# Kernel tuning notes

Measured on AMD Instinct MI355X. Metric: run time of the kernel, lower is better.

## Reference

```python
import jax, jax.numpy as jnp
import numpy as np

B, GNN_DIM, TR_DIM, F = 16384, 512, 768, 1024


def setup_inputs() -> dict:
    key = jax.random.key(0)
    ks = jax.random.split(key, 16)
    s = 0.02
    return {
        "gnn_features": jax.random.normal(ks[0], (B, GNN_DIM), jnp.float32),
        "transformer_features": jax.random.normal(ks[1], (B, TR_DIM), jnp.float32),
        # gnn_projector / transformer_projector (torch Linear: y = x @ W.T + b)
        "Wg": jax.random.normal(ks[2], (F, GNN_DIM), jnp.float32) * s,
        "bg": jnp.zeros((F,), jnp.float32),
        "Wt": jax.random.normal(ks[3], (F, TR_DIM), jnp.float32) * s,
        "bt": jnp.zeros((F,), jnp.float32),
        # MultiheadAttention value-projection slice of in_proj_weight and out_proj.
        # With seq_len==1 the softmax over a single key is identically 1, so the
        # attention output is exactly out_proj(v_proj(key)); Q/K projections do
        # not affect the output (their gradients are exactly zero).
        "Wv": jax.random.normal(ks[4], (F, F), jnp.float32) * s,
        "bv": jnp.zeros((F,), jnp.float32),
        "Wo": jax.random.normal(ks[5], (F, F), jnp.float32) * s,
        "bo": jnp.zeros((F,), jnp.float32),
        # fusion_layers: Linear(2F -> F), GELU, Dropout(eval: identity), Linear(F -> F)
        "W1": jax.random.normal(ks[6], (F, 2 * F), jnp.float32) * s,
        "b1": jnp.zeros((F,), jnp.float32),
        "W2": jax.random.normal(ks[7], (F, F), jnp.float32) * s,
        "b2": jnp.zeros((F,), jnp.float32),
    }


def reference(gnn_features, transformer_features, Wg, bg, Wt, bt, Wv, bv, Wo, bo, W1, b1, W2, b2):
    # projections to fusion space  [B, F]
    gnn_proj = gnn_features @ Wg.T + bg
    tr_proj = transformer_features @ Wt.T + bt
    # degenerate single-token cross-attention: softmax over 1 key == 1, so
    # attn(q, k, v=k) = out_proj(v_proj(k)) regardless of the query.
    gnn_attended = (tr_proj @ Wv.T + bv) @ Wo.T + bo   # attention(gnn_seq, tr_seq, tr_seq)
    tr_attended = (gnn_proj @ Wv.T + bv) @ Wo.T + bo   # attention(tr_seq, gnn_seq, gnn_seq)
    combined = jnp.concatenate([gnn_attended, tr_attended], axis=-1)  # [B, 2F]
    h = jax.nn.gelu(combined @ W1.T + b1, approximate=False)          # exact GELU (torch default)
    fused = h @ W2.T + b2
    return fused + gnn_proj + tr_proj
```

## Files before the change

### kernel.cpp

```cpp
#include <hip/hip_runtime.h>
#include <cmath>

#define GAS __attribute__((address_space(1)))
#define LAS __attribute__((address_space(3)))

typedef __bf16 bf16x8 __attribute__((ext_vector_type(8)));
typedef float f32x4 __attribute__((ext_vector_type(4)));

__device__ __forceinline__ void gload16(const void* g, void* l) {
    __builtin_amdgcn_global_load_lds((const GAS void*)g, (LAS void*)l, 16, 0, 0);
}

__global__ void k_prep_convert(const float* __restrict__ gnn, const float* __restrict__ tr,
                               const float* __restrict__ Wo, const float* __restrict__ W1,
                               const float* __restrict__ W2, const float* __restrict__ Wg,
                               const float* __restrict__ Wt,
                               __bf16* __restrict__ X, __bf16* __restrict__ Wo_b,
                               __bf16* __restrict__ W1ab, __bf16* __restrict__ Wp) {
    int b = blockIdx.x;
    const float* src; __bf16* dst; int sld, dld, base, c8;
    if (b < 4096)       { src = gnn;       sld = 512;  dst = X + 1024;        dld = 2304; base = 0;     c8 = 64; }
    else if (b < 10240) { src = tr;        sld = 768;  dst = X + 1536;        dld = 2304; base = 4096;  c8 = 96; }
    else if (b < 10752) { src = Wo;        sld = 1024; dst = Wo_b;            dld = 1024; base = 10240; c8 = 128; }
    else if (b < 11264) { src = W1;        sld = 2048; dst = W1ab;            dld = 1024; base = 10752; c8 = 128; }
    else if (b < 11776) { src = W1 + 1024; sld = 2048; dst = W1ab + 1024*1024; dld = 1024; base = 11264; c8 = 128; }
    else if (b < 12288) { src = W2;        sld = 1024; dst = Wp;              dld = 2304; base = 11776; c8 = 128; }
    else if (b < 12544) { src = Wg;        sld = 512;  dst = Wp + 1024;       dld = 2304; base = 12288; c8 = 64; }
    else                { src = Wt;        sld = 768;  dst = Wp + 1536;       dld = 2304; base = 12544; c8 = 96; }
    int idx = (b - base) * 256 + threadIdx.x;
    int r = idx / c8;
    int c = (idx - r * c8) << 3;
    const float4* s = reinterpret_cast<const float4*>(src + (long)r * sld + c);
    float4 x0 = s[0], x1 = s[1];
    bf16x8 v;
    v[0] = (__bf16)x0.x; v[1] = (__bf16)x0.y; v[2] = (__bf16)x0.z; v[3] = (__bf16)x0.w;
    v[4] = (__bf16)x1.x; v[5] = (__bf16)x1.y; v[6] = (__bf16)x1.z; v[7] = (__bf16)x1.w;
    *reinterpret_cast<bf16x8*>(dst + (long)r * dld + c) = v;
}

__global__ void k_prep_transpose(const float* __restrict__ Wv, const float* __restrict__ Wg,
                                 const float* __restrict__ Wt,
                                 __bf16* __restrict__ WvT, __bf16* __restrict__ WgT,
                                 __bf16* __restrict__ WtT) {
    __shared__ float t[32][33];
    int b = blockIdx.x;
    const float* src; __bf16* dst; int R, C, tile;
    if (b < 1024)      { src = Wv; dst = WvT; R = 1024; C = 1024; tile = b; }
    else if (b < 1536) { src = Wg; dst = WgT; R = 1024; C = 512;  tile = b - 1024; }
    else               { src = Wt; dst = WtT; R = 1024; C = 768;  tile = b - 1536; }
    int tx_n = C >> 5;
    int c0 = (tile % tx_n) << 5, r0 = (tile / tx_n) << 5;
    int tx = threadIdx.x, ty = threadIdx.y;
    #pragma unroll
    for (int i = 0; i < 32; i += 8)
        t[ty + i][tx] = src[(long)(r0 + ty + i) * C + c0 + tx];
    __syncthreads();
    #pragma unroll
    for (int i = 0; i < 32; i += 8)
        dst[(long)(c0 + ty + i) * R + r0 + tx] = (__bf16)t[tx][ty + i];
}

__global__ void k_bias_att(const float* __restrict__ Wo, const float* __restrict__ bv,
                           const float* __restrict__ bo, float* __restrict__ b_att) {
    int i = blockIdx.x;
    float s = 0.f;
    for (int k = threadIdx.x; k < 1024; k += 256) s += Wo[i * 1024 + k] * bv[k];
    __shared__ float red[256];
    red[threadIdx.x] = s;
    __syncthreads();
    for (int off = 128; off > 0; off >>= 1) {
        if (threadIdx.x < off) red[threadIdx.x] += red[threadIdx.x + off];
        __syncthreads();
    }
    if (threadIdx.x == 0) b_att[i] = red[0] + bo[i];
}

__global__ void k_bias_z2(const float* __restrict__ W1, const float* __restrict__ b_att,
                          const float* __restrict__ b1,
                          const __bf16* __restrict__ P, const __bf16* __restrict__ Q,
                          const float* __restrict__ bt, const float* __restrict__ bg,
                          const float* __restrict__ b2,
                          float* __restrict__ bz2, float* __restrict__ b_out) {
    int i = blockIdx.x;
    float s = 0.f;
    for (int k = threadIdx.x; k < 1024; k += 256) {
        s += (W1[(long)i * 2048 + k] + W1[(long)i * 2048 + 1024 + k]) * b_att[k];
        s += (float)P[i * 1024 + k] * bt[k];
        s += (float)Q[i * 1024 + k] * bg[k];
    }
    __shared__ float red[256];
    red[threadIdx.x] = s;
    __syncthreads();
    for (int off = 128; off > 0; off >>= 1) {
        if (threadIdx.x < off) red[threadIdx.x] += red[threadIdx.x + off];
        __syncthreads();
    }
    if (threadIdx.x == 0) {
        bz2[i] = red[0] + b1[i];
        b_out[i] = b2[i] + bg[i] + bt[i];
    }
}

template <int BM, int BN>
__global__ __launch_bounds__(256, 2) void k_gemm_nt(
    const __bf16* __restrict__ A, int lda,
    const __bf16* __restrict__ B, int ldb,
    __bf16* __restrict__ C, int ldc,
    int K, int n_tiles) {
    constexpr int BK = 32;
    constexpr int MR = BM / 32, NR = BN / 32;
    __shared__ alignas(16) __bf16 As[2][BM][BK];
    __shared__ alignas(16) __bf16 Bs[2][BN][BK];

    const int tid = threadIdx.x;
    const int lane = tid & 63;
    const int wave = tid >> 6;
    int bid = blockIdx.x;
    const int nwg = gridDim.x;
    if ((nwg & 7) == 0) bid = (bid & 7) * (nwg >> 3) + (bid >> 3);
    const int bn = bid % n_tiles;
    const int bm = bid / n_tiles;
    const int m0 = bm * BM, n0 = bn * BN;

    const int rp_l = tid >> 2;
    const int sp = tid & 3;

    const int wr = (wave >> 1) * (BM / 2);
    const int wc = (wave & 1) * (BN / 2);
    const int fr = lane & 15;
    const int fb = (lane >> 4) << 4;

    f32x4 acc[MR][NR] = {};
    const int nk = K / BK;

    auto stage = [&](int buf, int kt) {
        char* abase = (char*)&As[buf][0][0];
        char* bbase = (char*)&Bs[buf][0][0];
        #pragma unroll
        for (int it = 0; it < BM / 64; ++it) {
            int rp = it * 64 + rp_l;
            int rl = (rp & ~1) | ((rp ^ (rp >> 2)) & 1);
            int sl = sp ^ (rl & 3);
            gload16(A + (long)(m0 + rl) * lda + kt * BK + sl * 8,
                    abase + it * 4096 + tid * 16);
        }
        #pragma unroll
        for (int it = 0; it < BN / 64; ++it) {
            int rp = it * 64 + rp_l;
            int rl = (rp & ~1) | ((rp ^ (rp >> 2)) & 1);
            int sl = sp ^ (rl & 3);
            gload16(B + (long)(n0 + rl) * ldb + kt * BK + sl * 8,
                    bbase + it * 4096 + tid * 16);
        }
    };

    stage(0, 0);
    for (int kt = 0; kt < nk; ++kt) {
        const int buf = kt & 1;
        __syncthreads();
        if (kt + 1 < nk) stage(buf ^ 1, kt + 1);
        const char* abase = (const char*)&As[buf][0][0];
        const char* bbase = (const char*)&Bs[buf][0][0];
        bf16x8 af[MR], bfr[NR];
        #pragma unroll
        for (int m = 0; m < MR; ++m) {
            int r = wr + m * 16 + fr;
            af[m] = *(const bf16x8*)(abase + (((r << 6) + fb) ^ ((r & 7) << 4)));
        }
        #pragma unroll
        for (int n = 0; n < NR; ++n) {
            int r = wc + n * 16 + fr;
            bfr[n] = *(const bf16x8*)(bbase + (((r << 6) + fb) ^ ((r & 7) << 4)));
        }
        #pragma unroll
        for (int m = 0; m < MR; ++m)
            #pragma unroll
            for (int n = 0; n < NR; ++n)
                acc[m][n] = __builtin_amdgcn_mfma_f32_16x16x32_bf16(af[m], bfr[n], acc[m][n], 0, 0, 0);
    }

    const int r0 = (lane >> 4) << 2;
    #pragma unroll
    for (int n = 0; n < NR; ++n) {
        const int gc = n0 + wc + n * 16 + fr;
        #pragma unroll
        for (int m = 0; m < MR; ++m) {
            const long rbase = (long)(m0 + wr + m * 16 + r0);
            #pragma unroll
            for (int r = 0; r < 4; ++r)
                C[(rbase + r) * ldc + gc] = (__bf16)acc[m][n][r];
        }
    }
}

template <int MODE>
__device__ __forceinline__ void gemm8_body(
    const __bf16* __restrict__ A, int lda,
    const __bf16* __restrict__ B, int ldb,
    void* __restrict__ Cv, int ldc,
    const float* __restrict__ bias,
    int K, int n_tiles) {
    __shared__ __bf16 As[2][2][256][32];
    __shared__ __bf16 Bs[2][2][256][32];

    const int tid = threadIdx.x;
    const int lane = tid & 63;
    const int wave = tid >> 6;
    const int wm = wave >> 2;
    const int wn = wave & 3;

    int bid = blockIdx.x;
    const int nwg = gridDim.x;
    if ((nwg & 7) == 0) bid = (bid & 7) * (nwg >> 3) + (bid >> 3);
    const int bn = bid % n_tiles;
    const int bm = bid / n_tiles;
    const int m0 = bm * 256, n0 = bn * 256;

    const int rp0 = tid >> 2;
    const int rl0 = (rp0 & ~1) | ((rp0 ^ (rp0 >> 2)) & 1);
    const int slo = (tid & 3) ^ (rl0 & 3);
    const __bf16* Ag = A + (long)(m0 + rl0) * lda + slo * 8;
    const __bf16* Bg = B + (long)(n0 + rl0) * ldb + slo * 8;
    const long lda128 = (long)128 * lda;
    const long ldb128 = (long)128 * ldb;
    const int tid16 = tid * 16;

    const int fr = lane & 15;
    const int gb = (lane >> 4) << 4;

    f32x4 acc[8][4] = {};
    bf16x8 af[2][4];
    bf16x8 bfr[2][4];

    const int nk = K >> 6;
    const int NI = nk >> 1;

#define STAGE_A(PAR, KT, KH) { \
        char* l_ = (char*)&As[PAR][KH][0][0] + tid16; \
        const __bf16* g_ = Ag + (long)(KT) * 64 + (KH) * 32; \
        gload16(g_, l_); \
        gload16(g_ + lda128, l_ + 8192); }
#define STAGE_B(PAR, KT, KH) { \
        char* l_ = (char*)&Bs[PAR][KH][0][0] + tid16; \
        const __bf16* g_ = Bg + (long)(KT) * 64 + (KH) * 32; \
        gload16(g_, l_); \
        gload16(g_ + ldb128, l_ + 8192); }
#define VMC6 asm volatile("s_waitcnt vmcnt(6)" ::: "memory")
#define VMC4 asm volatile("s_waitcnt vmcnt(4)" ::: "memory")
#define VMC0 asm volatile("s_waitcnt vmcnt(0)" ::: "memory")
#define BAR  __builtin_amdgcn_s_barrier()
#define PIN  __builtin_amdgcn_sched_barrier(0)
#define RD_A(IDX, PAR, KS, MH) { \
        const char* a_ = (const char*)&As[PAR][KS][0][0]; \
        _Pragma("unroll") \
        for (int m_ = 0; m_ < 4; ++m_) { \
            int r_ = wm * 128 + (MH) * 64 + m_ * 16 + fr; \
            af[IDX][m_] = *(const bf16x8*)(a_ + (((r_ << 6) + gb) ^ ((r_ & 7) << 4))); } }
#define RD_B(IDX, PAR, KS) { \
        const char* b_ = (const char*)&Bs[PAR][KS][0][0]; \
        _Pragma("unroll") \
        for (int n_ = 0; n_ < 4; ++n_) { \
            int r_ = wn * 64 + n_ * 16 + fr; \
            bfr[IDX][n_] = *(const bf16x8*)(b_ + (((r_ << 6) + gb) ^ ((r_ & 7) << 4))); } }
#define MFMA16(AC, BC, MH) { \
        __builtin_amdgcn_s_setprio(1); \
        _Pragma("unroll") \
        for (int m_ = 0; m_ < 4; ++m_) { \
            _Pragma("unroll") \
            for (int n_ = 0; n_ < 4; ++n_) \
                acc[(MH) * 4 + m_][n_] = __builtin_amdgcn_mfma_f32_16x16x32_bf16( \
                    af[AC][m_], bfr[BC][n_], acc[(MH) * 4 + m_][n_], 0, 0, 0); } \
        __builtin_amdgcn_s_setprio(0); }

    STAGE_B(0, 0, 0); STAGE_A(0, 0, 0); STAGE_B(0, 0, 1); STAGE_A(0, 0, 1);
    STAGE_B(1, 1, 0); STAGE_A(1, 1, 0); STAGE_B(1, 1, 1);
    VMC4;
    BAR;
    RD_B(0, 0, 0); RD_A(0, 0, 0, 0);

    for (int I = 0; I < NI; ++I) {
        const int t = 2 * I;
        const bool nl = (I < NI - 1);
        STAGE_A(1, t + 1, 1);
        BAR; PIN; RD_A(1, 0, 0, 1); PIN;            MFMA16(0, 0, 0); BAR;
        if (nl) STAGE_B(0, t + 2, 0);
        BAR; PIN; RD_B(1, 0, 1); RD_A(0, 0, 1, 0); PIN; MFMA16(1, 0, 1); BAR;
        if (nl) STAGE_A(0, t + 2, 0);
        BAR; PIN; RD_A(1, 0, 1, 1); PIN;            MFMA16(0, 1, 0); BAR;
        if (nl) { STAGE_B(0, t + 2, 1); VMC6; } else { VMC0; }
        BAR; PIN; RD_B(0, 1, 0); RD_A(0, 1, 0, 0); PIN; MFMA16(1, 1, 1); BAR;
        if (nl) STAGE_A(0, t + 2, 1);
        BAR; PIN; RD_A(1, 1, 0, 1); PIN;            MFMA16(0, 0, 0); BAR;
        if (nl) STAGE_B(1, t + 3, 0);
        BAR; PIN; RD_B(1, 1, 1); RD_A(0, 1, 1, 0); PIN; MFMA16(1, 0, 1); BAR;
        if (nl) STAGE_A(1, t + 3, 0);
        BAR; PIN; RD_A(1, 1, 1, 1); PIN;            MFMA16(0, 1, 0); BAR;
        if (nl) { STAGE_B(1, t + 3, 1); VMC6; }
        BAR; PIN; RD_B(0, 0, 0); RD_A(0, 0, 0, 0); PIN; MFMA16(1, 1, 1); BAR;
    }
#undef MFMA16
#undef RD_B
#undef RD_A
#undef PIN
#undef BAR
#undef VMC0
#undef VMC4
#undef VMC6
#undef STAGE_B
#undef STAGE_A

    const int r0q = (lane >> 4) << 2;
    #pragma unroll
    for (int n = 0; n < 4; ++n) {
        const int gc = n0 + wn * 64 + n * 16 + fr;
        const float bval = bias ? bias[gc] : 0.0f;
        #pragma unroll
        for (int mq = 0; mq < 8; ++mq) {
            const long rbase = (long)(m0 + wm * 128 + mq * 16 + r0q);
            #pragma unroll
            for (int r = 0; r < 4; ++r) {
                float v = acc[mq][n][r] + bval;
                const long row = rbase + r;
                if (MODE == 1) {
                    float u = v * (0.7978845608f + 0.0356774081f * v * v);
                    float e = __expf(-2.0f * fabsf(u));
                    float th = (1.0f - e) / (1.0f + e);
                    th = copysignf(th, u);
                    v = 0.5f * v * (1.0f + th);
                    ((__bf16*)Cv)[row * ldc + gc] = (__bf16)v;
                } else {
                    ((float*)Cv)[row * ldc + gc] = v;
                }
            }
        }
    }
}

__global__ __launch_bounds__(512, 2) void k_gemm8_gelu(
    const __bf16* __restrict__ A, int lda, const __bf16* __restrict__ B, int ldb,
    void* __restrict__ Cv, int ldc, const float* __restrict__ bias, int K, int n_tiles) {
    gemm8_body<1>(A, lda, B, ldb, Cv, ldc, bias, K, n_tiles);
}
__global__ __launch_bounds__(512, 2) void k_gemm8_out(
    const __bf16* __restrict__ A, int lda, const __bf16* __restrict__ B, int ldb,
    void* __restrict__ Cv, int ldc, const float* __restrict__ bias, int K, int n_tiles) {
    gemm8_body<2>(A, lda, B, ldb, Cv, ldc, bias, K, n_tiles);
}

extern "C" void kernel_launch(void* const* d_in, const int* in_sizes, int n_in,
                              void* d_out, int out_size, void* d_ws, size_t ws_size,
                              hipStream_t stream) {
    constexpr int Bsz = 16384, F = 1024, GD = 512, TD = 768;
    constexpr int XLD = F + GD + TD;

    const float* gnn = (const float*)d_in[0];
    const float* tr  = (const float*)d_in[1];
    const float* Wg  = (const float*)d_in[2];
    const float* bg  = (const float*)d_in[3];
    const float* Wt  = (const float*)d_in[4];
    const float* bt  = (const float*)d_in[5];
    const float* Wv  = (const float*)d_in[6];
    const float* bv  = (const float*)d_in[7];
    const float* Wo  = (const float*)d_in[8];
    const float* bo  = (const float*)d_in[9];
    const float* W1  = (const float*)d_in[10];
    const float* b1  = (const float*)d_in[11];
    const float* W2  = (const float*)d_in[12];
    const float* b2  = (const float*)d_in[13];
    float* out = (float*)d_out;

    char* w = (char*)d_ws;
    auto alloc = [&](size_t bytes) {
        char* p = w;
        w += (bytes + 255) & ~(size_t)255;
        return p;
    };
    __bf16* X    = (__bf16*)alloc((size_t)Bsz * XLD * 2);
    __bf16* M1   = (__bf16*)alloc((size_t)F * (GD + TD) * 2);
    __bf16* Wp   = (__bf16*)alloc((size_t)F * XLD * 2);
    __bf16* WvT  = (__bf16*)alloc((size_t)F * F * 2);
    __bf16* WgT  = (__bf16*)alloc((size_t)GD * F * 2);
    __bf16* WtT  = (__bf16*)alloc((size_t)TD * F * 2);
    __bf16* Wo_b = (__bf16*)alloc((size_t)F * F * 2);
    __bf16* W1ab = (__bf16*)alloc((size_t)2 * F * F * 2);
    __bf16* AT   = (__bf16*)alloc((size_t)F * F * 2);
    __bf16* PQ   = (__bf16*)alloc((size_t)2 * F * F * 2);
    float* b_att = (float*)alloc(F * 4);
    float* bz2   = (float*)alloc(F * 4);
    float* b_out = (float*)alloc(F * 4);
    if ((size_t)(w - (char*)d_ws) > ws_size) return;

    dim3 b256(256);
    __bf16* P = PQ;
    __bf16* Q = PQ + (size_t)F * F;

    k_prep_convert<<<dim3(12928), b256, 0, stream>>>(gnn, tr, Wo, W1, W2, Wg, Wt,
                                                     X, Wo_b, W1ab, Wp);
    k_prep_transpose<<<dim3(2304), dim3(32, 8), 0, stream>>>(Wv, Wg, Wt, WvT, WgT, WtT);
    k_bias_att<<<dim3(F), b256, 0, stream>>>(Wo, bv, bo, b_att);

    k_gemm_nt<64, 64><<<dim3((F / 64) * (F / 64)), b256, 0, stream>>>(
        WvT, F, Wo_b, F, AT, F, F, F / 64);
    k_gemm_nt<64, 64><<<dim3((2 * F / 64) * (F / 64)), b256, 0, stream>>>(
        W1ab, F, AT, F, PQ, F, F, F / 64);
    k_gemm_nt<64, 64><<<dim3((F / 64) * (GD / 64)), b256, 0, stream>>>(
        Q, F, WgT, F, M1, GD + TD, F, GD / 64);
    k_gemm_nt<64, 64><<<dim3((F / 64) * (TD / 64)), b256, 0, stream>>>(
        P, F, WtT, F, M1 + GD, GD + TD, F, TD / 64);

    k_bias_z2<<<dim3(F), b256, 0, stream>>>(W1, b_att, b1, P, Q, bt, bg, b2, bz2, b_out);

    k_gemm8_gelu<<<dim3((Bsz / 256) * (F / 256)), dim3(512), 0, stream>>>(
        X + F, XLD, M1, GD + TD, X, XLD, bz2, GD + TD, F / 256);

    k_gemm8_out<<<dim3((Bsz / 256) * (F / 256)), dim3(512), 0, stream>>>(
        X, XLD, Wp, XLD, out, F, b_out, XLD, F / 256);
}
```

Measured before the change: 233.0 us.

## Restructure gemm8 LDS layout, staging schedule, and vectorize epilogue through LDS

```diff
diff --git a/kernel.cpp b/kernel.cpp
--- a/kernel.cpp
+++ b/kernel.cpp
@@ -200,8 +200,7 @@
     void* __restrict__ Cv, int ldc,
     const float* __restrict__ bias,
     int K, int n_tiles) {
-    __shared__ __bf16 As[2][2][256][32];
-    __shared__ __bf16 Bs[2][2][256][32];
+    __shared__ char lds[131072];
 
     const int tid = threadIdx.x;
     const int lane = tid & 63;
@@ -216,123 +215,144 @@
     const int bm = bid / n_tiles;
     const int m0 = bm * 256, n0 = bn * 256;
 
-    const int rp0 = tid >> 2;
-    const int rl0 = (rp0 & ~1) | ((rp0 ^ (rp0 >> 2)) & 1);
-    const int slo = (tid & 3) ^ (rl0 & 3);
-    const __bf16* Ag = A + (long)(m0 + rl0) * lda + slo * 8;
-    const __bf16* Bg = B + (long)(n0 + rl0) * ldb + slo * 8;
-    const long lda128 = (long)128 * lda;
-    const long ldb128 = (long)128 * ldb;
+    const int rowA = ((tid >> 7) << 4) + (tid & 15);
+    const int colA = (((tid >> 6) & 1) << 5) + (((tid >> 4) & 3) << 3);
+    const int rowB = ((tid >> 6) << 4) + (tid & 15);
+    const int colB = (((tid >> 4) & 3) << 3);
+    const __bf16* Ag = A + (long)(m0 + rowA) * lda + colA;
+    const __bf16* Bg = B + (long)(n0 + rowB) * ldb + colB;
     const int tid16 = tid * 16;
-
+    const int l16 = lane * 16;
     const int fr = lane & 15;
-    const int gb = (lane >> 4) << 4;
+
+    const int bnh = wn >> 1;
+    const int bno = (wn & 1) * 4096;
 
     f32x4 acc[8][4] = {};
-    bf16x8 af[2][4];
+    bf16x8 af[4];
     bf16x8 bfr[2][4];
 
     const int nk = K >> 6;
     const int NI = nk >> 1;
 
-#define STAGE_A(PAR, KT, KH) { \
-        char* l_ = (char*)&As[PAR][KH][0][0] + tid16; \
-        const __bf16* g_ = Ag + (long)(KT) * 64 + (KH) * 32; \
-        gload16(g_, l_); \
-        gload16(g_ + lda128, l_ + 8192); }
-#define STAGE_B(PAR, KT, KH) { \
-        char* l_ = (char*)&Bs[PAR][KH][0][0] + tid16; \
-        const __bf16* g_ = Bg + (long)(KT) * 64 + (KH) * 32; \
-        gload16(g_, l_); \
-        gload16(g_ + ldb128, l_ + 8192); }
+#define STAGE_A(PAR, KT, MH, QH) \
+    gload16(Ag + (long)(KT) * 64 + (long)((MH) * 128 + (QH) * 64) * lda, \
+            lds + (PAR) * 32768 + (MH) * 16384 + (QH) * 8192 + tid16)
+#define STAGE_B(PAR, KT, NH, KK) \
+    gload16(Bg + (long)(KT) * 64 + (KK) * 32 + (long)((NH) * 128) * ldb, \
+            lds + 65536 + (PAR) * 32768 + (NH) * 16384 + (KK) * 8192 + tid16)
+#define VMC8 asm volatile("s_waitcnt vmcnt(8)" ::: "memory")
 #define VMC6 asm volatile("s_waitcnt vmcnt(6)" ::: "memory")
-#define VMC4 asm volatile("s_waitcnt vmcnt(4)" ::: "memory")
 #define VMC0 asm volatile("s_waitcnt vmcnt(0)" ::: "memory")
 #define BAR  __builtin_amdgcn_s_barrier()
-#define PIN  __builtin_amdgcn_sched_barrier(0)
-#define RD_A(IDX, PAR, KS, MH) { \
-        const char* a_ = (const char*)&As[PAR][KS][0][0]; \
+#define RD_A4(PAR, QH, KK) { \
+        const char* a_ = lds + (PAR) * 32768 + wm * 16384 + (QH) * 8192 + (KK) * 1024; \
         _Pragma("unroll") \
-        for (int m_ = 0; m_ < 4; ++m_) { \
-            int r_ = wm * 128 + (MH) * 64 + m_ * 16 + fr; \
-            af[IDX][m_] = *(const bf16x8*)(a_ + (((r_ << 6) + gb) ^ ((r_ & 7) << 4))); } }
-#define RD_B(IDX, PAR, KS) { \
-        const char* b_ = (const char*)&Bs[PAR][KS][0][0]; \
+        for (int m_ = 0; m_ < 4; ++m_) \
+            af[m_] = *(const bf16x8*)(a_ + m_ * 2048 + l16); }
+#define RD_B4(KK, PAR) { \
+        const char* b_ = lds + 65536 + (PAR) * 32768 + bnh * 16384 + (KK) * 8192 + bno; \
         _Pragma("unroll") \
-        for (int n_ = 0; n_ < 4; ++n_) { \
-            int r_ = wn * 64 + n_ * 16 + fr; \
-            bfr[IDX][n_] = *(const bf16x8*)(b_ + (((r_ << 6) + gb) ^ ((r_ & 7) << 4))); } }
-#define MFMA16(AC, BC, MH) { \
+        for (int n_ = 0; n_ < 4; ++n_) \
+            bfr[KK][n_] = *(const bf16x8*)(b_ + n_ * 1024 + l16); }
+#define MFMA16(QH, KK) { \
         __builtin_amdgcn_s_setprio(1); \
         _Pragma("unroll") \
         for (int m_ = 0; m_ < 4; ++m_) { \
             _Pragma("unroll") \
             for (int n_ = 0; n_ < 4; ++n_) \
-                acc[(MH) * 4 + m_][n_] = __builtin_amdgcn_mfma_f32_16x16x32_bf16( \
-                    af[AC][m_], bfr[BC][n_], acc[(MH) * 4 + m_][n_], 0, 0, 0); } \
+                acc[(QH) * 4 + m_][n_] = __builtin_amdgcn_mfma_f32_16x16x32_bf16( \
+                    af[m_], bfr[KK][n_], acc[(QH) * 4 + m_][n_], 0, 0, 0); } \
         __builtin_amdgcn_s_setprio(0); }
 
-    STAGE_B(0, 0, 0); STAGE_A(0, 0, 0); STAGE_B(0, 0, 1); STAGE_A(0, 0, 1);
-    STAGE_B(1, 1, 0); STAGE_A(1, 1, 0); STAGE_B(1, 1, 1);
-    VMC4;
-    BAR;
-    RD_B(0, 0, 0); RD_A(0, 0, 0, 0);
+    STAGE_A(0, 0, 0, 0); STAGE_A(0, 0, 1, 0);
+    STAGE_B(0, 0, 0, 0); STAGE_B(0, 0, 1, 0);
+    STAGE_A(0, 0, 0, 1); STAGE_A(0, 0, 1, 1);
+    STAGE_B(0, 0, 0, 1); STAGE_B(0, 0, 1, 1);
+    STAGE_A(1, 1, 0, 0); STAGE_A(1, 1, 1, 0);
+    STAGE_B(1, 1, 0, 0); STAGE_B(1, 1, 1, 0);
 
     for (int I = 0; I < NI; ++I) {
         const int t = 2 * I;
-        const bool nl = (I < NI - 1);
-        STAGE_A(1, t + 1, 1);
-        BAR; PIN; RD_A(1, 0, 0, 1); PIN;            MFMA16(0, 0, 0); BAR;
-        if (nl) STAGE_B(0, t + 2, 0);
-        BAR; PIN; RD_B(1, 0, 1); RD_A(0, 0, 1, 0); PIN; MFMA16(1, 0, 1); BAR;
-        if (nl) STAGE_A(0, t + 2, 0);
-        BAR; PIN; RD_A(1, 0, 1, 1); PIN;            MFMA16(0, 1, 0); BAR;
-        if (nl) { STAGE_B(0, t + 2, 1); VMC6; } else { VMC0; }
-        BAR; PIN; RD_B(0, 1, 0); RD_A(0, 1, 0, 0); PIN; MFMA16(1, 1, 1); BAR;
-        if (nl) STAGE_A(0, t + 2, 1);
-        BAR; PIN; RD_A(1, 1, 0, 1); PIN;            MFMA16(0, 0, 0); BAR;
-        if (nl) STAGE_B(1, t + 3, 0);
-        BAR; PIN; RD_B(1, 1, 1); RD_A(0, 1, 1, 0); PIN; MFMA16(1, 0, 1); BAR;
-        if (nl) STAGE_A(1, t + 3, 0);
-        BAR; PIN; RD_A(1, 1, 1, 1); PIN;            MFMA16(0, 1, 0); BAR;
-        if (nl) { STAGE_B(1, t + 3, 1); VMC6; }
-        BAR; PIN; RD_B(0, 0, 0); RD_A(0, 0, 0, 0); PIN; MFMA16(1, 1, 1); BAR;
+        const bool nl = (I + 1 < NI);
+        VMC8;
+        STAGE_A(1, t + 1, 0, 1); STAGE_A(1, t + 1, 1, 1);
+        BAR; RD_B4(0, 0); RD_A4(0, 0, 0); MFMA16(0, 0); BAR;
+        VMC6;
+        STAGE_B(1, t + 1, 0, 1); STAGE_B(1, t + 1, 1, 1);
+        BAR; RD_B4(1, 0); RD_A4(0, 0, 1); MFMA16(0, 1); BAR;
+        if (nl) { STAGE_A(0, t + 2, 0, 0); STAGE_A(0, t + 2, 1, 0); } else { VMC0; }
+        BAR; RD_A4(0, 1, 0); MFMA16(1, 0); BAR;
+        if (nl) { STAGE_B(0, t + 2, 0, 0); STAGE_B(0, t + 2, 1, 0); }
+        BAR; RD_A4(0, 1, 1); MFMA16(1, 1); BAR;
+        VMC8;
+        if (nl) { STAGE_A(0, t + 2, 0, 1); STAGE_A(0, t + 2, 1, 1); }
+        BAR; RD_B4(0, 1); RD_A4(1, 0, 0); MFMA16(0, 0); BAR;
+        VMC6;
+        if (nl) { STAGE_B(0, t + 2, 0, 1); STAGE_B(0, t + 2, 1, 1); }
+        BAR; RD_B4(1, 1); RD_A4(1, 0, 1); MFMA16(0, 1); BAR;
+        if (nl) { STAGE_A(1, t + 3, 0, 0); STAGE_A(1, t + 3, 1, 0); }
+        BAR; RD_A4(1, 1, 0); MFMA16(1, 0); BAR;
+        if (nl) { STAGE_B(1, t + 3, 0, 0); STAGE_B(1, t + 3, 1, 0); }
+        BAR; RD_A4(1, 1, 1); MFMA16(1, 1); BAR;
     }
 #undef MFMA16
-#undef RD_B
-#undef RD_A
-#undef PIN
+#undef RD_B4
+#undef RD_A4
 #undef BAR
 #undef VMC0
-#undef VMC4
 #undef VMC6
+#undef VMC8
 #undef STAGE_B
 #undef STAGE_A
 
+    char* scr = lds + wave * 16384;
+    float bval[4];
+    #pragma unroll
+    for (int n_ = 0; n_ < 4; ++n_)
+        bval[n_] = bias ? bias[n0 + wn * 64 + n_ * 16 + fr] : 0.0f;
     const int r0q = (lane >> 4) << 2;
+
     #pragma unroll
-    for (int n = 0; n < 4; ++n) {
-        const int gc = n0 + wn * 64 + n * 16 + fr;
-        const float bval = bias ? bias[gc] : 0.0f;
-        #pragma unroll
-        for (int mq = 0; mq < 8; ++mq) {
-            const long rbase = (long)(m0 + wm * 128 + mq * 16 + r0q);
+    for (int mq = 0; mq < 8; ++mq) {
+        #pragma unroll
+        for (int n_ = 0; n_ < 4; ++n_) {
             #pragma unroll
             for (int r = 0; r < 4; ++r) {
-                float v = acc[mq][n][r] + bval;
-                const long row = rbase + r;
+                float v = acc[mq][n_][r] + bval[n_];
                 if (MODE == 1) {
                     float u = v * (0.7978845608f + 0.0356774081f * v * v);
                     float e = __expf(-2.0f * fabsf(u));
                     float th = (1.0f - e) / (1.0f + e);
                     th = copysignf(th, u);
                     v = 0.5f * v * (1.0f + th);
-                    ((__bf16*)Cv)[row * ldc + gc] = (__bf16)v;
-                } else {
-                    ((float*)Cv)[row * ldc + gc] = v;
                 }
+                *(float*)(scr + (r0q + r) * 272 + (n_ * 16 + fr) * 4) = v;
             }
         }
+        __builtin_amdgcn_s_waitcnt(0);
+        if (MODE == 2) {
+            #pragma unroll
+            for (int rep = 0; rep < 4; ++rep) {
+                int row = rep * 4 + (lane >> 4);
+                f32x4 val = *(const f32x4*)(scr + row * 272 + (lane & 15) * 16);
+                long grow = (long)(m0 + wm * 128 + mq * 16 + row);
+                *(f32x4*)&((float*)Cv)[grow * ldc + n0 + wn * 64 + (lane & 15) * 4] = val;
+            }
+        } else {
+            #pragma unroll
+            for (int rep = 0; rep < 2; ++rep) {
+                int row = rep * 8 + (lane >> 3);
+                f32x4 v0 = *(const f32x4*)(scr + row * 272 + (lane & 7) * 32);
+                f32x4 v1 = *(const f32x4*)(scr + row * 272 + (lane & 7) * 32 + 16);
+                bf16x8 o;
+                o[0] = (__bf16)v0[0]; o[1] = (__bf16)v0[1]; o[2] = (__bf16)v0[2]; o[3] = (__bf16)v0[3];
+                o[4] = (__bf16)v1[0]; o[5] = (__bf16)v1[1]; o[6] = (__bf16)v1[2]; o[7] = (__bf16)v1[3];
+                long grow = (long)(m0 + wm * 128 + mq * 16 + row);
+                *(bf16x8*)&((__bf16*)Cv)[grow * ldc + n0 + wn * 64 + (lane & 7) * 8] = o;
+            }
+        }
+        __builtin_amdgcn_s_waitcnt(0);
     }
 }
 
```

Measured after the change: 225.9 us. 1.03x faster.
